# Kernel optimization log

Measured on AMD Instinct MI355X. Metric: run time of the kernel, lower is better.

Reference implementation:

```python
import jax, jax.numpy as jnp
import numpy as np
from jax import lax

FREQ, TIME = 8, 8
TSLOTS, NUM_AP = 8, 4
N_DEV = 8192
E_DD, E_DA, E_AD = 262144, 32768, 32768
HID = 64


def _w(key, shape):
    fan_in = shape[0] if len(shape) == 2 else int(np.prod(shape[1:]))
    return jax.random.normal(key, shape, jnp.float32) / np.sqrt(fan_in)


def setup_inputs() -> dict:
    key = jax.random.key(0)
    ks = iter(jax.random.split(key, 64))
    inp = {}
    inp['device_pos'] = jax.random.normal(next(ks), (N_DEV, 2), jnp.float32)
    inp['ap_pos'] = jax.random.normal(next(ks), (NUM_AP, 2), jnp.float32)
    inp['csi'] = jax.random.normal(next(ks), (N_DEV, NUM_AP, FREQ, TIME, 2), jnp.float32)
    inp['node_packets'] = jax.random.randint(next(ks), (N_DEV,), 0, 100, jnp.int32)
    inp['dd_src'] = jax.random.randint(next(ks), (E_DD,), 0, N_DEV, jnp.int32)
    inp['dd_dst'] = jax.random.randint(next(ks), (E_DD,), 0, N_DEV, jnp.int32)
    inp['da_src'] = jax.random.randint(next(ks), (E_DA,), 0, N_DEV, jnp.int32)
    inp['da_dst'] = jax.random.randint(next(ks), (E_DA,), 0, NUM_AP, jnp.int32)
    inp['ad_src'] = jax.random.randint(next(ks), (E_AD,), 0, NUM_AP, jnp.int32)
    inp['ad_dst'] = jax.random.randint(next(ks), (E_AD,), 0, N_DEV, jnp.int32)
    # CSIEncoder params
    inp['cnn1_W'] = _w(next(ks), (16, 2, 3, 3)); inp['cnn1_b'] = jnp.zeros((16,), jnp.float32)
    inp['cnn2_W'] = _w(next(ks), (32, 16, 3, 3)); inp['cnn2_b'] = jnp.zeros((32,), jnp.float32)
    inp['csi_fc_W'] = _w(next(ks), (32 * FREQ * TIME, HID)); inp['csi_fc_b'] = jnp.zeros((HID,), jnp.float32)
    # DeviceEncoder params
    inp['dev_pos_W'] = _w(next(ks), (3, 16)); inp['dev_pos_b'] = jnp.zeros((16,), jnp.float32)
    inp['dev_csi_W'] = _w(next(ks), (NUM_AP * HID, 64)); inp['dev_csi_b'] = jnp.zeros((64,), jnp.float32)
    inp['dev_merge_W'] = _w(next(ks), (80, 64)); inp['dev_merge_b'] = jnp.zeros((64,), jnp.float32)
    # APEncoder params
    inp['ap_enc_W'] = _w(next(ks), (2, 64)); inp['ap_enc_b'] = jnp.zeros((64,), jnp.float32)
    # 2 hetero layers x 3 relations GraphConv(64,64)
    for name in ['g1_dd', 'g1_da', 'g1_ad', 'g2_dd', 'g2_da', 'g2_ad']:
        inp[name + '_W'] = _w(next(ks), (64, 64))
        inp[name + '_b'] = jnp.zeros((64,), jnp.float32)
    # ap_head (sched_head is defined but unused in the original forward)
    inp['aph1_W'] = _w(next(ks), (64, 64)); inp['aph1_b'] = jnp.zeros((64,), jnp.float32)
    inp['aph2_W'] = _w(next(ks), (64, TSLOTS * NUM_AP)); inp['aph2_b'] = jnp.zeros((TSLOTS * NUM_AP,), jnp.float32)
    return inp


def _conv2d(x, W, b):
    y = lax.conv_general_dilated(x, W, (1, 1), 'SAME', dimension_numbers=('NCHW', 'OIHW', 'NCHW'))
    return y + b[None, :, None, None]


def _graph_conv(x_src, src, dst, n_src, n_dst, W, b):
    # DGL GraphConv, norm='both': x/sqrt(out_deg) -> scatter-sum -> /sqrt(in_deg) -> linear
    ones = jnp.ones(src.shape[0], x_src.dtype)
    deg_out = jnp.maximum(jax.ops.segment_sum(ones, src, num_segments=n_src), 1.0)
    deg_in = jnp.maximum(jax.ops.segment_sum(ones, dst, num_segments=n_dst), 1.0)
    m = (x_src * lax.rsqrt(deg_out)[:, None])[src]            # gather per edge
    agg = jax.ops.segment_sum(m, dst, num_segments=n_dst)      # scatter-sum to dst
    agg = agg * lax.rsqrt(deg_in)[:, None]
    return agg @ W + b


def reference(device_pos, ap_pos, csi, node_packets, dd_src, dd_dst, da_src, da_dst, ad_src, ad_dst,
              cnn1_W, cnn1_b, cnn2_W, cnn2_b, csi_fc_W, csi_fc_b,
              dev_pos_W, dev_pos_b, dev_csi_W, dev_csi_b, dev_merge_W, dev_merge_b,
              ap_enc_W, ap_enc_b,
              g1_dd_W, g1_dd_b, g1_da_W, g1_da_b, g1_ad_W, g1_ad_b,
              g2_dd_W, g2_dd_b, g2_da_W, g2_da_b, g2_ad_W, g2_ad_b,
              aph1_W, aph1_b, aph2_W, aph2_b):
    N, AP = csi.shape[0], csi.shape[1]
    # CSIEncoder (per-AP loop vectorized as a single batched conv over N*AP)
    x = csi.reshape(N * AP, FREQ, TIME, 2).transpose(0, 3, 1, 2)   # [N*AP,2,F,T]
    x = jax.nn.relu(_conv2d(x, cnn1_W, cnn1_b))
    x = jax.nn.relu(_conv2d(x, cnn2_W, cnn2_b))
    x = x.reshape(N * AP, -1)                                      # [N*AP, 32*F*T]
    csi_embed = jax.nn.relu(x @ csi_fc_W + csi_fc_b).reshape(N, AP * HID)
    # DeviceEncoder
    pin = jnp.concatenate([device_pos, node_packets.astype(jnp.float32)[:, None]], axis=1)
    pos_f = jax.nn.relu(pin @ dev_pos_W + dev_pos_b)
    csi_f = jax.nn.relu(csi_embed @ dev_csi_W + dev_csi_b)
    h_dev = jax.nn.relu(jnp.concatenate([pos_f, csi_f], axis=1) @ dev_merge_W + dev_merge_b)
    # APEncoder
    h_ap = jax.nn.relu(ap_pos @ ap_enc_W + ap_enc_b)
    # HeteroGraphConv layer 1 (aggregate='sum' across relations sharing dst type)
    hd1 = (_graph_conv(h_dev, dd_src, dd_dst, N, N, g1_dd_W, g1_dd_b)
           + _graph_conv(h_ap, ad_src, ad_dst, NUM_AP, N, g1_ad_W, g1_ad_b))
    ha1 = _graph_conv(h_dev, da_src, da_dst, N, NUM_AP, g1_da_W, g1_da_b)
    hd1, ha1 = jax.nn.relu(hd1), jax.nn.relu(ha1)
    # HeteroGraphConv layer 2
    hd2 = (_graph_conv(hd1, dd_src, dd_dst, N, N, g2_dd_W, g2_dd_b)
           + _graph_conv(ha1, ad_src, ad_dst, NUM_AP, N, g2_ad_W, g2_ad_b))
    hd2 = jax.nn.relu(hd2)
    # ap_head -> [N, T, A]
    ap_logits = (jax.nn.relu(hd2 @ aph1_W + aph1_b) @ aph2_W + aph2_b).reshape(N, TSLOTS, NUM_AP)
    logits_AP = ap_logits.transpose(2, 1, 0)                       # [A,T,N]
    # eval branch: deterministic softmax + argmax one-hot over devices
    ap_soft_AP = jax.nn.softmax(logits_AP, axis=-1)
    idx = jnp.argmax(logits_AP, axis=-1)                           # [A,T]
    ap_onehot_AP = jax.nn.one_hot(idx, N, dtype=logits_AP.dtype)   # [A,T,N]
    ap_onehot_final = ap_onehot_AP.transpose(2, 1, 0)              # [N,T,A]
    sched_soft = ap_soft_AP.sum(axis=0).T                          # [N,T]
    sched_hard = (ap_onehot_final.sum(axis=-1) > 0).astype(jnp.float32)
    return (sched_hard, ap_logits, sched_soft)
```

## Files before the change

kernel.cpp:

```cpp
#include <hip/hip_runtime.h>

#define NDEV 8192
#define NAP  4
#define NSAMP 32768
#define EDD 262144
#define EDA 32768
#define EAD 32768
#define CHUNK 8192
#define KC 128
#define ASTR2 132

typedef float vf2 __attribute__((ext_vector_type(2)));
static __device__ __forceinline__ vf2 pk_fma(vf2 a, vf2 b, vf2 c) {
    return __builtin_elementwise_fma(a, b, c);
}

using sh8 = __attribute__((ext_vector_type(8))) short;
using f32x4 = __attribute__((ext_vector_type(4))) float;
using f32x16 = __attribute__((ext_vector_type(16))) float;

static __device__ __forceinline__ unsigned short bf16_rtne(float f) {
    unsigned u = __float_as_uint(f);
    u += 0x7fffu + ((u >> 16) & 1u);
    return (unsigned short)(u >> 16);
}
static __device__ __forceinline__ float bf16f(unsigned short h) {
    return __uint_as_float(((unsigned)h) << 16);
}

__global__ void repack_kernel(const float* __restrict__ w2, float* __restrict__ wpk,
                              const float* __restrict__ w1, float* __restrict__ w1p,
                              const float* __restrict__ fcW, uint4* __restrict__ wfc,
                              const float* __restrict__ Wc, uint4* __restrict__ wcc)
{
    int i = blockIdx.x * 256 + threadIdx.x;
    if (i < 1152) {
        int lane = i & 63, s = (i >> 6) & 1, tap = i >> 7;
        int oc = lane & 31, g = lane >> 5;
        unsigned int d[4];
        #pragma unroll
        for (int d4 = 0; d4 < 4; ++d4) {
            unsigned short u01[2];
            #pragma unroll
            for (int h = 0; h < 2; ++h) {
                int e = 2 * d4 + h;
                int ic = g * 8 + e;
                float v = w2[oc * 144 + ic * 9 + tap];
                unsigned short hi = bf16_rtne(v);
                u01[h] = (s == 0) ? hi : bf16_rtne(v - bf16f(hi));
            }
            d[d4] = (unsigned)u01[0] | ((unsigned)u01[1] << 16);
        }
        ((uint4*)wpk)[i] = make_uint4(d[0], d[1], d[2], d[3]);
    }
    int j = i - 4608;
    if (j >= 0 && j < 288) {
        int h = j & 1, v = j >> 1;
        int o2 = v & 7, r = v >> 3;
        w1p[j] = w1[(2 * o2 + h) * 18 + r];
    }
    int h1 = i - 5120;
    if (h1 >= 0 && h1 < 32768) {
        int s = h1 & 1, l = (h1 >> 1) & 63, nt = (h1 >> 7) & 3, kstep = h1 >> 9;
        unsigned int d[4];
        #pragma unroll
        for (int d4 = 0; d4 < 4; ++d4) {
            unsigned short u01[2];
            #pragma unroll
            for (int hh = 0; hh < 2; ++hh) {
                int e = 2 * d4 + hh;
                int k = kstep * 32 + (l >> 4) * 8 + e;
                int n = nt * 16 + (l & 15);
                float v = fcW[(long)k * 64 + n];
                unsigned short hi = bf16_rtne(v);
                u01[hh] = (s == 0) ? hi : bf16_rtne(v - bf16f(hi));
            }
            d[d4] = (unsigned)u01[0] | ((unsigned)u01[1] << 16);
        }
        wfc[h1] = make_uint4(d[0], d[1], d[2], d[3]);
    }
    int h2 = i - 37888;
    if (h2 >= 0 && h2 < 4096) {
        int s = h2 & 1, l = (h2 >> 1) & 63, nt = (h2 >> 7) & 3, kstep = h2 >> 9;
        unsigned int d[4];
        #pragma unroll
        for (int d4 = 0; d4 < 4; ++d4) {
            unsigned short u01[2];
            #pragma unroll
            for (int hh = 0; hh < 2; ++hh) {
                int e = 2 * d4 + hh;
                int k = kstep * 32 + (l >> 4) * 8 + e;
                int n = nt * 16 + (l & 15);
                float v = Wc[(long)k * 64 + n];
                unsigned short hi = bf16_rtne(v);
                u01[hh] = (s == 0) ? hi : bf16_rtne(v - bf16f(hi));
            }
            d[d4] = (unsigned)u01[0] | ((unsigned)u01[1] << 16);
        }
        wcc[h2] = make_uint4(d[0], d[1], d[2], d[3]);
    }
}

__global__ __launch_bounds__(256) void conv_kernel(
    const float* __restrict__ csi,
    float* __restrict__ c2,
    const float* __restrict__ w1p, const float* __restrict__ b1,
    const float* __restrict__ wpk, const float* __restrict__ b2)
{
    __shared__ float sw1p[288];
    __shared__ float sb1[16];
    __shared__ float sb2[32];
    __shared__ float inpad[4][2][10][10];
    __shared__ __align__(16) unsigned short c1h[15360];
    const int tid = threadIdx.x;

    for (int i = tid; i < 288; i += 256) sw1p[i] = w1p[i];
    if (tid < 16) sb1[tid] = b1[tid];
    if (tid < 32) sb2[tid] = b2[tid];
    float* ip = &inpad[0][0][0][0];
    for (int i = tid; i < 800; i += 256) ip[i] = 0.f;
    unsigned int* cz = (unsigned int*)c1h;
    for (int i = tid; i < 7680; i += 256) cz[i] = 0u;
    __syncthreads();

    const long s0 = (long)blockIdx.x * 4;
    for (int i = tid; i < 512; i += 256) {
        int si = i >> 7, r = i & 127;
        int f = r >> 4, t = (r >> 1) & 7, c = r & 1;
        inpad[si][c][f + 1][t + 1] = csi[s0 * 128 + i];
    }
    __syncthreads();

    {
        const int si1 = tid >> 6, p1 = tid & 63;
        const int f1 = p1 >> 3, t1 = p1 & 7;
        float inv[18];
        #pragma unroll
        for (int ic = 0; ic < 2; ++ic)
            #pragma unroll
            for (int df = 0; df < 3; ++df)
                #pragma unroll
                for (int dt = 0; dt < 3; ++dt)
                    inv[ic * 9 + df * 3 + dt] = inpad[si1][ic][f1 + df][t1 + dt];
        vf2 a1[8];
        #pragma unroll
        for (int o2 = 0; o2 < 8; ++o2) a1[o2] = (vf2){sb1[2 * o2], sb1[2 * o2 + 1]};
        const vf2* sw1v = (const vf2*)sw1p;
        #pragma unroll
        for (int r = 0; r < 18; ++r) {
            vf2 xv = {inv[r], inv[r]};
            #pragma unroll
            for (int o2 = 0; o2 < 8; ++o2)
                a1[o2] = pk_fma(xv, sw1v[r * 8 + o2], a1[o2]);
        }
        float v[16];
        #pragma unroll
        for (int o2 = 0; o2 < 8; ++o2) {
            v[2 * o2]     = fmaxf(a1[o2].x, 0.f);
            v[2 * o2 + 1] = fmaxf(a1[o2].y, 0.f);
        }
        const int cell = ((f1 + 1) * 12 + (t1 + 1)) * 8;
        #pragma unroll
        for (int g = 0; g < 2; ++g) {
            unsigned int hd[4], ld[4];
            #pragma unroll
            for (int d = 0; d < 4; ++d) {
                float x0 = v[g * 8 + 2 * d], x1 = v[g * 8 + 2 * d + 1];
                unsigned short h0 = bf16_rtne(x0), h1 = bf16_rtne(x1);
                unsigned short l0 = bf16_rtne(x0 - bf16f(h0));
                unsigned short l1 = bf16_rtne(x1 - bf16f(h1));
                hd[d] = (unsigned)h0 | ((unsigned)h1 << 16);
                ld[d] = (unsigned)l0 | ((unsigned)l1 << 16);
            }
            *(uint4*)&c1h[(si1 * 4 + g) * 960 + cell]     = make_uint4(hd[0], hd[1], hd[2], hd[3]);
            *(uint4*)&c1h[(si1 * 4 + 2 + g) * 960 + cell] = make_uint4(ld[0], ld[1], ld[2], ld[3]);
        }
    }

    const int lane = tid & 63;
    sh8 Bh[9], Bl[9];
    {
        const sh8* bfp = (const sh8*)wpk;
        #pragma unroll
        for (int tap = 0; tap < 9; ++tap) {
            Bh[tap] = bfp[(tap * 2 + 0) * 64 + lane];
            Bl[tap] = bfp[(tap * 2 + 1) * 64 + lane];
        }
    }
    __syncthreads();

    const int w = __builtin_amdgcn_readfirstlane(tid >> 6);
    const int rr = lane & 31, g = lane >> 5;
    const float bias = sb2[rr];
    f32x16 acc0, acc1;
    #pragma unroll
    for (int u = 0; u < 16; ++u) { acc0[u] = bias; acc1[u] = bias; }

    const int p0f = rr >> 3, pt = rr & 7;
    const int p1f = 4 + p0f;
    const int hb = (w * 4 + g) * 960;
    const int lb = (w * 4 + 2 + g) * 960;

    #pragma unroll
    for (int df = 0; df < 3; ++df) {
        #pragma unroll
        for (int dt = 0; dt < 3; ++dt) {
            const int tap = df * 3 + dt;
            const int c0 = ((p0f + df) * 12 + (pt + dt)) * 8;
            const int c1i = ((p1f + df) * 12 + (pt + dt)) * 8;
            sh8 Ah0 = *(const sh8*)&c1h[hb + c0];
            sh8 Al0 = *(const sh8*)&c1h[lb + c0];
            sh8 Ah1 = *(const sh8*)&c1h[hb + c1i];
            sh8 Al1 = *(const sh8*)&c1h[lb + c1i];
            acc0 = __builtin_amdgcn_mfma_f32_32x32x16_bf16(Ah0, Bh[tap], acc0, 0, 0, 0);
            acc1 = __builtin_amdgcn_mfma_f32_32x32x16_bf16(Ah1, Bh[tap], acc1, 0, 0, 0);
            acc0 = __builtin_amdgcn_mfma_f32_32x32x16_bf16(Ah0, Bl[tap], acc0, 0, 0, 0);
            acc1 = __builtin_amdgcn_mfma_f32_32x32x16_bf16(Ah1, Bl[tap], acc1, 0, 0, 0);
            acc0 = __builtin_amdgcn_mfma_f32_32x32x16_bf16(Al0, Bh[tap], acc0, 0, 0, 0);
            acc1 = __builtin_amdgcn_mfma_f32_32x32x16_bf16(Al1, Bh[tap], acc1, 0, 0, 0);
        }
    }

    float* cb = &c2[(s0 + w) * 2048 + (long)rr * 64];
    #pragma unroll
    for (int qq = 0; qq < 4; ++qq) {
        float4 o;
        o.x = fmaxf(acc0[4 * qq + 0], 0.f); o.y = fmaxf(acc0[4 * qq + 1], 0.f);
        o.z = fmaxf(acc0[4 * qq + 2], 0.f); o.w = fmaxf(acc0[4 * qq + 3], 0.f);
        *(float4*)&cb[8 * qq + 4 * g] = o;
    }
    #pragma unroll
    for (int qq = 0; qq < 4; ++qq) {
        float4 o;
        o.x = fmaxf(acc1[4 * qq + 0], 0.f); o.y = fmaxf(acc1[4 * qq + 1], 0.f);
        o.z = fmaxf(acc1[4 * qq + 2], 0.f); o.w = fmaxf(acc1[4 * qq + 3], 0.f);
        *(float4*)&cb[32 + 8 * qq + 4 * g] = o;
    }
}

__global__ __launch_bounds__(256) void fc16_kernel(
    const float* __restrict__ A, const uint4* __restrict__ Wfrag,
    const float* __restrict__ bias, float* __restrict__ out, int K)
{
    __shared__ __align__(16) float smem[4224];
    float* As = smem;
    const int tid = threadIdx.x;
    const long m0g = (long)blockIdx.x * 16;
    const int ks = tid >> 6;
    const int lane = tid & 63;
    const int mrow = lane & 15;
    const int g = lane >> 4;

    f32x4 acc[4];
    #pragma unroll
    for (int nt = 0; nt < 4; ++nt) acc[nt] = (f32x4){0.f, 0.f, 0.f, 0.f};

    for (int kc = 0; kc < K; kc += KC) {
        __syncthreads();
        #pragma unroll
        for (int i = 0; i < 2; ++i) {
            int idx = tid + i * 256;
            int m = idx >> 5, kq = idx & 31;
            float4 v = *(const float4*)&A[(m0g + m) * K + kc + kq * 4];
            *(float4*)&As[m * ASTR2 + kq * 4] = v;
        }
        __syncthreads();
        const int kstep = (kc >> 5) + ks;
        const uint4* bp = Wfrag + (size_t)kstep * 512 + lane * 2;
        uint4 bh0 = bp[0],   bl0 = bp[1];
        uint4 bh1 = bp[128], bl1 = bp[129];
        uint4 bh2 = bp[256], bl2 = bp[257];
        uint4 bh3 = bp[384], bl3 = bp[385];
        const float4 a0 = *(const float4*)&As[mrow * ASTR2 + ks * 32 + g * 8];
        const float4 a1 = *(const float4*)&As[mrow * ASTR2 + ks * 32 + g * 8 + 4];
        float av[8] = {a0.x, a0.y, a0.z, a0.w, a1.x, a1.y, a1.z, a1.w};
        unsigned short hs[8], lss[8];
        #pragma unroll
        for (int e = 0; e < 8; ++e) {
            hs[e] = bf16_rtne(av[e]);
            lss[e] = bf16_rtne(av[e] - bf16f(hs[e]));
        }
        sh8 Ah = {(short)hs[0], (short)hs[1], (short)hs[2], (short)hs[3],
                  (short)hs[4], (short)hs[5], (short)hs[6], (short)hs[7]};
        sh8 Al = {(short)lss[0], (short)lss[1], (short)lss[2], (short)lss[3],
                  (short)lss[4], (short)lss[5], (short)lss[6], (short)lss[7]};
        #define FCMM(ntv, bhv, blv) \
            acc[ntv] = __builtin_amdgcn_mfma_f32_16x16x32_bf16(Ah, *(const sh8*)&(bhv), acc[ntv], 0, 0, 0); \
            acc[ntv] = __builtin_amdgcn_mfma_f32_16x16x32_bf16(Ah, *(const sh8*)&(blv), acc[ntv], 0, 0, 0); \
            acc[ntv] = __builtin_amdgcn_mfma_f32_16x16x32_bf16(Al, *(const sh8*)&(bhv), acc[ntv], 0, 0, 0);
        FCMM(0, bh0, bl0)
        FCMM(1, bh1, bl1)
        FCMM(2, bh2, bl2)
        FCMM(3, bh3, bl3)
        #undef FCMM
    }
    __syncthreads();
    float* red = smem;
    #pragma unroll
    for (int nt = 0; nt < 4; ++nt)
        #pragma unroll
        for (int r = 0; r < 4; ++r)
            red[(ks * 16 + g * 4 + r) * 64 + nt * 16 + mrow] = acc[nt][r];
    __syncthreads();
    {
        int m = tid >> 4, oq = tid & 15;
        float4 r0 = *(float4*)&red[(0 * 16 + m) * 64 + oq * 4];
        float4 r1 = *(float4*)&red[(1 * 16 + m) * 64 + oq * 4];
        float4 r2 = *(float4*)&red[(2 * 16 + m) * 64 + oq * 4];
        float4 r3 = *(float4*)&red[(3 * 16 + m) * 64 + oq * 4];
        const float4 b4 = *(const float4*)&bias[oq * 4];
        float4 o4;
        o4.x = fmaxf(r0.x + r1.x + r2.x + r3.x + b4.x, 0.f);
        o4.y = fmaxf(r0.y + r1.y + r2.y + r3.y + b4.y, 0.f);
        o4.z = fmaxf(r0.z + r1.z + r2.z + r3.z + b4.z, 0.f);
        o4.w = fmaxf(r0.w + r1.w + r2.w + r3.w + b4.w, 0.f);
        *(float4*)&out[(m0g + m) * 64 + oq * 4] = o4;
    }
}

__global__ __launch_bounds__(256) void merge_kernel(
    const float* __restrict__ dpos, const int* __restrict__ pkts,
    const float* __restrict__ csif,
    const float* __restrict__ Wp, const float* __restrict__ bp,
    const float* __restrict__ Wm, const float* __restrict__ bm,
    const int* __restrict__ degout,
    float* __restrict__ hdev, float* __restrict__ xn,
    const float* __restrict__ appos, const float* __restrict__ Wap,
    const float* __restrict__ bap, const int* __restrict__ degapo,
    float* __restrict__ hap, float* __restrict__ xnap)
{
    __shared__ float sWm[80][64];
    __shared__ float spos[4][16];
    __shared__ float scf[4][64];
    const int tid = threadIdx.x;
    for (int i = tid; i < 5120; i += 256) sWm[i >> 6][i & 63] = Wm[i];
    const int n0 = blockIdx.x * 4;
    (&scf[0][0])[tid] = csif[(long)n0 * 64 + tid];
    if (tid < 64) {
        int dl = tid >> 4, o = tid & 15;
        int d = n0 + dl;
        float px = dpos[d * 2], py = dpos[d * 2 + 1], pk = (float)pkts[d];
        float v = bp[o] + px * Wp[o] + py * Wp[16 + o] + pk * Wp[32 + o];
        spos[dl][o] = fmaxf(v, 0.f);
    }
    __syncthreads();
    const int o = tid & 63, dl = tid >> 6;
    float h = bm[o];
    #pragma unroll
    for (int j = 0; j < 16; ++j) h += spos[dl][j] * sWm[j][o];
    #pragma unroll 8
    for (int j = 0; j < 64; ++j) h += scf[dl][j] * sWm[16 + j][o];
    h = fmaxf(h, 0.f);
    const long idx = (long)(n0 + dl) * 64 + o;
    hdev[idx] = h;
    xn[idx] = h * rsqrtf(fmaxf((float)degout[n0 + dl], 1.f));
    if (blockIdx.x == 0) {
        int a = tid >> 6, oo = tid & 63;
        float v = fmaxf(bap[oo] + appos[a * 2] * Wap[oo] + appos[a * 2 + 1] * Wap[64 + oo], 0.f);
        hap[tid] = v;
        xnap[tid] = v * rsqrtf(fmaxf((float)degapo[a], 1.f));
    }
}

__global__ __launch_bounds__(256) void degrees_kernel(
    const int* __restrict__ dd_src, const int* __restrict__ dd_dst,
    const int* __restrict__ da_src, const int* __restrict__ da_dst,
    const int* __restrict__ ad_src, const int* __restrict__ ad_dst,
    int* deg_dd_out, int* deg_dd_in, int* deg_da_out, int* deg_ad_in, int* deg_small)
{
    __shared__ int s4[16];
    const int tid = threadIdx.x;
    if (tid < 16) s4[tid] = 0;
    __syncthreads();
    const int gid = blockIdx.x * 256 + tid;
    atomicAdd(&deg_dd_out[dd_src[gid]], 1);
    atomicAdd(&deg_dd_in[dd_dst[gid]], 1);
    if (gid < EDA) {
        atomicAdd(&deg_da_out[da_src[gid]], 1);
        atomicAdd(&s4[da_dst[gid]], 1);
        atomicAdd(&s4[8 + ad_src[gid]], 1);
        atomicAdd(&deg_ad_in[ad_dst[gid]], 1);
    }
    __syncthreads();
    if (tid < 16 && s4[tid] != 0) atomicAdd(&deg_small[tid], s4[tid]);
}

__global__ __launch_bounds__(1024) void scan_kernel(
    const int* __restrict__ degA, int* rsA, int* curA,
    const int* __restrict__ degB, int* rsB, int* curB)
{
    const int* deg = blockIdx.x ? degB : degA;
    int* rs = blockIdx.x ? rsB : rsA;
    int* cur = blockIdx.x ? curB : curA;
    __shared__ int sd[1024];
    const int tid = threadIdx.x;
    const int base = tid * 8;
    int v[8]; int s = 0;
    #pragma unroll
    for (int j = 0; j < 8; ++j) { v[j] = deg[base + j]; s += v[j]; }
    sd[tid] = s;
    __syncthreads();
    for (int off = 1; off < 1024; off <<= 1) {
        int t = (tid >= off) ? sd[tid - off] : 0;
        __syncthreads();
        sd[tid] += t;
        __syncthreads();
    }
    int ex = sd[tid] - s;
    #pragma unroll
    for (int j = 0; j < 8; ++j) { rs[base + j] = ex; cur[base + j] = ex; ex += v[j]; }
}

__global__ __launch_bounds__(256) void reorder_kernel(
    const int* __restrict__ src, const int* __restrict__ dst,
    int* __restrict__ cursor, int* __restrict__ ssrc, int nE)
{
    int e = blockIdx.x * 256 + threadIdx.x;
    if (e < nE) {
        int pos = atomicAdd(&cursor[dst[e]], 1);
        ssrc[pos] = src[e];
    }
}

__global__ __launch_bounds__(256) void gatherx_kernel(
    const int* __restrict__ rsdd, const int* __restrict__ degddi,
    const int* __restrict__ ssdd, const float* __restrict__ xn, float* __restrict__ aggdd,
    const int* __restrict__ rsad, const int* __restrict__ degadi,
    const int* __restrict__ ssad, const float* __restrict__ xnap, float* __restrict__ aggad,
    const int* __restrict__ da_src, const int* __restrict__ da_dst,
    const float* __restrict__ hdev, const int* __restrict__ degdao,
    float* __restrict__ aggda)
{
    __shared__ float sacc[4][64];
    const int b = blockIdx.x;
    const int tid = threadIdx.x;
    if (b < 1024) {
        const bool isdd = b < 512;
        const int lane = tid & 63;
        const int gbase = lane & 48;
        const int lg = lane & 15;
        const int fq = lg * 4;
        const int d = (isdd ? b : b - 512) * 16 + (tid >> 4);
        const int* rs = isdd ? rsdd : rsad;
        const int* dg = isdd ? degddi : degadi;
        const int* ss = isdd ? ssdd : ssad;
        const float* x = isdd ? xn : xnap;
        float* agg = isdd ? aggdd : aggad;
        const int start = rs[d], len = dg[d];
        float ax = 0.f, ay = 0.f, az = 0.f, aw = 0.f;
        for (int j = 0; j < len; j += 16) {
            const int rem = min(16, len - j);
            const int myidx = ss[start + j + min(lg, rem - 1)];
            float4 v[16];
            #pragma unroll
            for (int k = 0; k < 16; ++k) {
                const int sk = __shfl(myidx, gbase + min(k, rem - 1), 64);
                v[k] = *(const float4*)&x[(long)sk * 64 + fq];
            }
            #pragma unroll
            for (int k = 0; k < 16; ++k) {
                const float m = (k < rem) ? 1.f : 0.f;
                ax += m * v[k].x; ay += m * v[k].y;
                az += m * v[k].z; aw += m * v[k].w;
            }
        }
        const float sc = rsqrtf(fmaxf((float)len, 1.f));
        float4 o;
        o.x = ax * sc; o.y = ay * sc; o.z = az * sc; o.w = aw * sc;
        *(float4*)&agg[(long)d * 64 + fq] = o;
    } else {
        (&sacc[0][0])[tid] = 0.f;
        __syncthreads();
        const int f = tid & 63;
        const int base = (b - 1024) * 128;
        for (int e = base + (tid >> 6); e < base + 128; e += 4) {
            int s = da_src[e], d = da_dst[e];
            float sc = rsqrtf(fmaxf((float)degdao[s], 1.f));
            atomicAdd(&sacc[d][f], hdev[(long)s * 64 + f] * sc);
        }
        __syncthreads();
        float v = (&sacc[0][0])[tid];
        if (v != 0.f) atomicAdd(&aggda[tid], v);
    }
}

__global__ __launch_bounds__(256) void combinex_kernel(
    const float* __restrict__ agg1, const float* __restrict__ W1, const float* __restrict__ b1,
    const float* __restrict__ agg2, const float* __restrict__ W2, const float* __restrict__ b2,
    const int* __restrict__ degout, float* __restrict__ out, float* __restrict__ xnout,
    const float* __restrict__ aggda, const int* __restrict__ degdai,
    const float* __restrict__ Wda, const float* __restrict__ bda,
    const int* __restrict__ degapo, float* __restrict__ ha_out, float* __restrict__ ha_xn)
{
    __shared__ float sW1[64][64];
    __shared__ float sW2[64][64];
    __shared__ float sa1[4][64];
    __shared__ float sa2[4][64];
    const int tid = threadIdx.x;
    if (blockIdx.x < 2048) {
        for (int i = tid; i < 4096; i += 256) { sW1[i >> 6][i & 63] = W1[i]; sW2[i >> 6][i & 63] = W2[i]; }
        const int n0 = blockIdx.x * 4;
        (&sa1[0][0])[tid] = agg1[(long)n0 * 64 + tid];
        (&sa2[0][0])[tid] = agg2[(long)n0 * 64 + tid];
        __syncthreads();
        const int o = tid & 63, dl = tid >> 6;
        float acc1 = 0.f, acc2 = 0.f;
        #pragma unroll 8
        for (int k = 0; k < 64; ++k) {
            acc1 += sa1[dl][k] * sW1[k][o];
            acc2 += sa2[dl][k] * sW2[k][o];
        }
        float h = fmaxf(acc1 + acc2 + b1[o] + b2[o], 0.f);
        const long idx = (long)(n0 + dl) * 64 + o;
        out[idx] = h;
        if (xnout) xnout[idx] = h * rsqrtf(fmaxf((float)degout[n0 + dl], 1.f));
    } else {
        const int o = tid & 63, a = tid >> 6;
        float acc = 0.f;
        for (int k = 0; k < 64; ++k) acc += aggda[a * 64 + k] * Wda[k * 64 + o];
        float r = rsqrtf(fmaxf((float)degdai[a], 1.f));
        float h = fmaxf(acc * r + bda[o], 0.f);
        ha_out[tid] = h;
        ha_xn[tid] = h * rsqrtf(fmaxf((float)degapo[a], 1.f));
    }
}

__global__ __launch_bounds__(256) void head_kernel(
    const float* __restrict__ hd2,
    const float* __restrict__ W1, const float* __restrict__ b1,
    const float* __restrict__ W2, const float* __restrict__ b2,
    float* __restrict__ logits_out)
{
    __shared__ float sW1[64][64];
    __shared__ float sW2[64][32];
    __shared__ float sh[4][64];
    __shared__ float st[4][64];
    const int tid = threadIdx.x;
    for (int i = tid; i < 4096; i += 256) sW1[i >> 6][i & 63] = W1[i];
    for (int i = tid; i < 2048; i += 256) sW2[i >> 5][i & 31] = W2[i];
    const int n0 = blockIdx.x * 4;
    (&sh[0][0])[tid] = hd2[(long)n0 * 64 + tid];
    __syncthreads();
    const int o = tid & 63, dl = tid >> 6;
    float acc = b1[o];
    #pragma unroll 8
    for (int k = 0; k < 64; ++k) acc += sh[dl][k] * sW1[k][o];
    st[dl][o] = fmaxf(acc, 0.f);
    __syncthreads();
    if (tid < 128) {
        int j = tid & 31, d2 = tid >> 5;
        float a2 = b2[j];
        #pragma unroll 8
        for (int k = 0; k < 64; ++k) a2 += st[d2][k] * sW2[k][j];
        logits_out[(long)(n0 + d2) * 32 + j] = a2;
    }
}

__global__ __launch_bounds__(1024) void softmax_stats_kernel(
    const float* __restrict__ logits,
    float* __restrict__ smax, int* __restrict__ sargm, float* __restrict__ ssum)
{
    __shared__ float smx[1024];
    __shared__ int sid[1024];
    __shared__ float ssm[1024];
    const int j = blockIdx.x;
    const int tid = threadIdx.x;
    float best = -__builtin_inff(); int bid = 0x7fffffff;
    for (int n = tid; n < NDEV; n += 1024) {
        float v = logits[n * 32 + j];
        if (v > best) { best = v; bid = n; }
    }
    smx[tid] = best; sid[tid] = bid;
    __syncthreads();
    for (int s = 512; s > 0; s >>= 1) {
        if (tid < s) {
            float v2 = smx[tid + s]; int i2 = sid[tid + s];
            if (v2 > smx[tid] || (v2 == smx[tid] && i2 < sid[tid])) { smx[tid] = v2; sid[tid] = i2; }
        }
        __syncthreads();
    }
    const float mx = smx[0];
    float part = 0.f;
    for (int n = tid; n < NDEV; n += 1024) part += expf(logits[n * 32 + j] - mx);
    ssm[tid] = part;
    __syncthreads();
    for (int s = 512; s > 0; s >>= 1) {
        if (tid < s) ssm[tid] += ssm[tid + s];
        __syncthreads();
    }
    if (tid == 0) { smax[j] = mx; sargm[j] = sid[0]; ssum[j] = ssm[0]; }
}

__global__ __launch_bounds__(256) void final_kernel(
    const float* __restrict__ logits, const float* __restrict__ smax,
    const int* __restrict__ sargm, const float* __restrict__ ssum,
    float* __restrict__ hard, float* __restrict__ soft)
{
    const int gid = blockIdx.x * 256 + threadIdx.x;
    const int n = gid >> 3, t = gid & 7;
    float s = 0.f; int h = 0;
    #pragma unroll
    for (int a = 0; a < 4; ++a) {
        int j = t * 4 + a;
        s += expf(logits[n * 32 + j] - smax[j]) / ssum[j];
        h |= (sargm[j] == n) ? 1 : 0;
    }
    hard[gid] = (float)h;
    soft[gid] = s;
}

extern "C" void kernel_launch(void* const* d_in, const int* in_sizes, int n_in,
                              void* d_out, int out_size, void* d_ws, size_t ws_size,
                              hipStream_t stream)
{
    const float* device_pos = (const float*)d_in[0];
    const float* ap_pos     = (const float*)d_in[1];
    const float* csi        = (const float*)d_in[2];
    const int*   node_pk    = (const int*)d_in[3];
    const int* dd_src = (const int*)d_in[4];
    const int* dd_dst = (const int*)d_in[5];
    const int* da_src = (const int*)d_in[6];
    const int* da_dst = (const int*)d_in[7];
    const int* ad_src = (const int*)d_in[8];
    const int* ad_dst = (const int*)d_in[9];
    const float* w1  = (const float*)d_in[10]; const float* b1  = (const float*)d_in[11];
    const float* w2  = (const float*)d_in[12]; const float* b2  = (const float*)d_in[13];
    const float* fcW = (const float*)d_in[14]; const float* fcb = (const float*)d_in[15];
    const float* Wp  = (const float*)d_in[16]; const float* bp  = (const float*)d_in[17];
    const float* Wc  = (const float*)d_in[18]; const float* bc  = (const float*)d_in[19];
    const float* Wm  = (const float*)d_in[20]; const float* bm  = (const float*)d_in[21];
    const float* Wap = (const float*)d_in[22]; const float* bap = (const float*)d_in[23];
    const float* g1ddW = (const float*)d_in[24]; const float* g1ddb = (const float*)d_in[25];
    const float* g1daW = (const float*)d_in[26]; const float* g1dab = (const float*)d_in[27];
    const float* g1adW = (const float*)d_in[28]; const float* g1adb = (const float*)d_in[29];
    const float* g2ddW = (const float*)d_in[30]; const float* g2ddb = (const float*)d_in[31];
    const float* g2adW = (const float*)d_in[34]; const float* g2adb = (const float*)d_in[35];
    const float* a1W = (const float*)d_in[36]; const float* a1b = (const float*)d_in[37];
    const float* a2W = (const float*)d_in[38]; const float* a2b = (const float*)d_in[39];

    float* ws = (float*)d_ws;
    size_t o_c2    = 0;
    size_t o_emb   = o_c2 + (size_t)CHUNK * 2048;
    size_t o_csif  = o_emb + (size_t)NSAMP * 64;
    size_t o_hdev  = o_csif + (size_t)NDEV * 64;
    size_t o_hap   = o_hdev + (size_t)NDEV * 64;
    size_t o_hd1   = o_hap + 256;
    size_t o_ha1   = o_hd1 + (size_t)NDEV * 64;
    size_t o_hd2   = o_ha1 + 256;
    size_t o_aggdd = o_hd2 + (size_t)NDEV * 64;
    size_t o_aggad = o_aggdd + (size_t)NDEV * 64;
    size_t o_xn    = o_aggad + (size_t)NDEV * 64;
    size_t o_xnap  = o_xn + (size_t)NDEV * 64;
    size_t o_wpk   = o_xnap + 256;
    size_t o_w1p   = o_wpk + 4608;
    size_t o_wfc   = o_w1p + 288;
    size_t o_wcc   = o_wfc + 131072;
    size_t o_zero  = o_wcc + 16384;
    size_t o_degddo = o_zero;
    size_t o_degddi = o_degddo + NDEV;
    size_t o_degdao = o_degddi + NDEV;
    size_t o_degadi = o_degdao + NDEV;
    size_t o_degsm  = o_degadi + NDEV;
    size_t o_aggda  = o_degsm + 16;
    size_t o_zend   = o_aggda + 256;
    size_t o_rsdd  = o_zend;
    size_t o_curdd = o_rsdd + NDEV;
    size_t o_rsad  = o_curdd + NDEV;
    size_t o_curad = o_rsad + NDEV;
    size_t o_ssdd  = o_curad + NDEV;
    size_t o_ssad  = o_ssdd + EDD;
    size_t o_smax  = o_ssad + EAD;
    size_t o_ssum  = o_smax + 32;
    size_t o_sargm = o_ssum + 32;

    float* out = (float*)d_out;
    float* out_hard   = out;
    float* out_logits = out + 65536;
    float* out_soft   = out + 65536 + 262144;

    hipMemsetAsync((void*)(ws + o_zero), 0, (o_zend - o_zero) * sizeof(float), stream);
    repack_kernel<<<164, 256, 0, stream>>>(w2, ws + o_wpk, w1, ws + o_w1p,
                                           fcW, (uint4*)(ws + o_wfc),
                                           Wc, (uint4*)(ws + o_wcc));

    degrees_kernel<<<EDD / 256, 256, 0, stream>>>(dd_src, dd_dst, da_src, da_dst, ad_src, ad_dst,
                                                  (int*)(ws + o_degddo), (int*)(ws + o_degddi),
                                                  (int*)(ws + o_degdao), (int*)(ws + o_degadi),
                                                  (int*)(ws + o_degsm));
    scan_kernel<<<2, 1024, 0, stream>>>((int*)(ws + o_degddi), (int*)(ws + o_rsdd), (int*)(ws + o_curdd),
                                        (int*)(ws + o_degadi), (int*)(ws + o_rsad), (int*)(ws + o_curad));
    reorder_kernel<<<EDD / 256, 256, 0, stream>>>(dd_src, dd_dst, (int*)(ws + o_curdd),
                                                  (int*)(ws + o_ssdd), EDD);
    reorder_kernel<<<EAD / 256, 256, 0, stream>>>(ad_src, ad_dst, (int*)(ws + o_curad),
                                                  (int*)(ws + o_ssad), EAD);

    for (int c = 0; c < NSAMP / CHUNK; ++c) {
        const float* csi_c = csi + (size_t)c * CHUNK * 128;
        float* emb_c = ws + o_emb + (size_t)c * CHUNK * 64;
        conv_kernel<<<CHUNK / 4, 256, 0, stream>>>(csi_c, ws + o_c2, ws + o_w1p, b1, ws + o_wpk, b2);
        fc16_kernel<<<CHUNK / 16, 256, 0, stream>>>(ws + o_c2, (const uint4*)(ws + o_wfc),
                                                    fcb, emb_c, 2048);
    }

    fc16_kernel<<<NDEV / 16, 256, 0, stream>>>(ws + o_emb, (const uint4*)(ws + o_wcc),
                                               bc, ws + o_csif, 256);
    merge_kernel<<<NDEV / 4, 256, 0, stream>>>(device_pos, node_pk, ws + o_csif,
                                               Wp, bp, Wm, bm, (int*)(ws + o_degddo),
                                               ws + o_hdev, ws + o_xn,
                                               ap_pos, Wap, bap, (int*)(ws + o_degsm) + 8,
                                               ws + o_hap, ws + o_xnap);

    gatherx_kernel<<<1280, 256, 0, stream>>>((int*)(ws + o_rsdd), (int*)(ws + o_degddi),
                                             (int*)(ws + o_ssdd), ws + o_xn, ws + o_aggdd,
                                             (int*)(ws + o_rsad), (int*)(ws + o_degadi),
                                             (int*)(ws + o_ssad), ws + o_xnap, ws + o_aggad,
                                             da_src, da_dst, ws + o_hdev,
                                             (int*)(ws + o_degdao), ws + o_aggda);
    combinex_kernel<<<2049, 256, 0, stream>>>(ws + o_aggdd, g1ddW, g1ddb,
                                              ws + o_aggad, g1adW, g1adb,
                                              (int*)(ws + o_degddo), ws + o_hd1, ws + o_xn,
                                              ws + o_aggda, (int*)(ws + o_degsm),
                                              g1daW, g1dab, (int*)(ws + o_degsm) + 8,
                                              ws + o_ha1, ws + o_xnap);

    gatherx_kernel<<<1024, 256, 0, stream>>>((int*)(ws + o_rsdd), (int*)(ws + o_degddi),
                                             (int*)(ws + o_ssdd), ws + o_xn, ws + o_aggdd,
                                             (int*)(ws + o_rsad), (int*)(ws + o_degadi),
                                             (int*)(ws + o_ssad), ws + o_xnap, ws + o_aggad,
                                             da_src, da_dst, ws + o_hd1,
                                             (int*)(ws + o_degdao), ws + o_aggda);
    combinex_kernel<<<2048, 256, 0, stream>>>(ws + o_aggdd, g2ddW, g2ddb,
                                              ws + o_aggad, g2adW, g2adb,
                                              (int*)(ws + o_degddo), ws + o_hd2, nullptr,
                                              nullptr, nullptr, nullptr, nullptr,
                                              nullptr, nullptr, nullptr);

    head_kernel<<<NDEV / 4, 256, 0, stream>>>(ws + o_hd2, a1W, a1b, a2W, a2b, out_logits);

    softmax_stats_kernel<<<32, 1024, 0, stream>>>(out_logits, ws + o_smax,
                                                  (int*)(ws + o_sargm), ws + o_ssum);
    final_kernel<<<65536 / 256, 256, 0, stream>>>(out_logits, ws + o_smax,
                                                  (int*)(ws + o_sargm), ws + o_ssum,
                                                  out_hard, out_soft);
    (void)in_sizes; (void)n_in; (void)out_size; (void)ws_size;
}
```

Baseline: 516.4 us.

## Fuse CSI conv and FC layers into one kernel keeping conv output in LDS

Replaces the chunked conv_kernel and fc16_kernel launches with a single convfc kernel. Each 512-thread block handles 16 samples, keeps the conv2 activations in a large shared-memory buffer in position-major layout, and runs the 2048x64 FC with split-K across waves followed by an LDS reduction. The FC weight repack is permuted to match the new activation layout. This removes the global round trip of the 2048-wide intermediate and several launches, at the cost of about 135KB of LDS per block, which limits occupancy to one block per CU.

```diff
diff --git a/kernel.cpp b/kernel.cpp
--- a/kernel.cpp
+++ b/kernel.cpp
@@ -6,7 +6,6 @@
 #define EDD 262144
 #define EDA 32768
 #define EAD 32768
-#define CHUNK 8192
 #define KC 128
 #define ASTR2 132
 
@@ -69,9 +68,10 @@
             #pragma unroll
             for (int hh = 0; hh < 2; ++hh) {
                 int e = 2 * d4 + hh;
-                int k = kstep * 32 + (l >> 4) * 8 + e;
+                int kp = kstep * 32 + (l >> 4) * 8 + e;
+                int korig = (kp & 31) * 64 + (kp >> 5);
                 int n = nt * 16 + (l & 15);
-                float v = fcW[(long)k * 64 + n];
+                float v = fcW[(long)korig * 64 + n];
                 unsigned short hi = bf16_rtne(v);
                 u01[hh] = (s == 0) ? hi : bf16_rtne(v - bf16f(hi));
             }
@@ -101,38 +101,52 @@
     }
 }
 
-__global__ __launch_bounds__(256) void conv_kernel(
+#define C2STR 2052
+__global__ __launch_bounds__(512) void convfc_kernel(
     const float* __restrict__ csi,
-    float* __restrict__ c2,
     const float* __restrict__ w1p, const float* __restrict__ b1,
-    const float* __restrict__ wpk, const float* __restrict__ b2)
-{
+    const float* __restrict__ wpk, const float* __restrict__ b2,
+    const uint4* __restrict__ wfc, const float* __restrict__ fcb,
+    float* __restrict__ emb)
+{
+    __shared__ __align__(16) char smem[135680];
     __shared__ float sw1p[288];
     __shared__ float sb1[16];
     __shared__ float sb2[32];
-    __shared__ float inpad[4][2][10][10];
-    __shared__ __align__(16) unsigned short c1h[15360];
+    __shared__ float sbF[64];
+    float* inpad = (float*)smem;
+    unsigned short* c1h = (unsigned short*)(smem + 12800);
+    float* c2h = (float*)smem;
+    float* red = (float*)smem;
     const int tid = threadIdx.x;
-
-    for (int i = tid; i < 288; i += 256) sw1p[i] = w1p[i];
+    const int lane = tid & 63;
+    const int w = __builtin_amdgcn_readfirstlane(tid >> 6);
+
+    for (int i = tid; i < 288; i += 512) sw1p[i] = w1p[i];
     if (tid < 16) sb1[tid] = b1[tid];
     if (tid < 32) sb2[tid] = b2[tid];
-    float* ip = &inpad[0][0][0][0];
-    for (int i = tid; i < 800; i += 256) ip[i] = 0.f;
-    unsigned int* cz = (unsigned int*)c1h;
-    for (int i = tid; i < 7680; i += 256) cz[i] = 0u;
-    __syncthreads();
-
-    const long s0 = (long)blockIdx.x * 4;
-    for (int i = tid; i < 512; i += 256) {
+    if (tid < 64) sbF[tid] = fcb[tid];
+    {
+        const uint4 z4 = make_uint4(0u, 0u, 0u, 0u);
+        uint4* ip4 = (uint4*)inpad;
+        for (int i = tid; i < 800; i += 512) ip4[i] = z4;
+        uint4* c14 = (uint4*)c1h;
+        for (int i = tid; i < 15360; i += 512) c14[i] = z4;
+    }
+    __syncthreads();
+
+    const long s0 = (long)blockIdx.x * 16;
+    for (int i = tid; i < 2048; i += 512) {
         int si = i >> 7, r = i & 127;
         int f = r >> 4, t = (r >> 1) & 7, c = r & 1;
-        inpad[si][c][f + 1][t + 1] = csi[s0 * 128 + i];
-    }
-    __syncthreads();
-
-    {
-        const int si1 = tid >> 6, p1 = tid & 63;
+        inpad[si * 200 + c * 100 + (f + 1) * 10 + (t + 1)] = csi[s0 * 128 + i];
+    }
+    __syncthreads();
+
+    #pragma unroll
+    for (int it = 0; it < 2; ++it) {
+        const int si1 = it * 8 + w;
+        const int p1 = lane;
         const int f1 = p1 >> 3, t1 = p1 & 7;
         float inv[18];
         #pragma unroll
@@ -141,7 +155,8 @@
             for (int df = 0; df < 3; ++df)
                 #pragma unroll
                 for (int dt = 0; dt < 3; ++dt)
-                    inv[ic * 9 + df * 3 + dt] = inpad[si1][ic][f1 + df][t1 + dt];
+                    inv[ic * 9 + df * 3 + dt] =
+                        inpad[si1 * 200 + ic * 100 + (f1 + df) * 10 + (t1 + dt)];
         vf2 a1[8];
         #pragma unroll
         for (int o2 = 0; o2 < 8; ++o2) a1[o2] = (vf2){sb1[2 * o2], sb1[2 * o2 + 1]};
@@ -177,7 +192,6 @@
         }
     }
 
-    const int lane = tid & 63;
     sh8 Bh[9], Bl[9];
     {
         const sh8* bfp = (const sh8*)wpk;
@@ -189,52 +203,106 @@
     }
     __syncthreads();
 
-    const int w = __builtin_amdgcn_readfirstlane(tid >> 6);
     const int rr = lane & 31, g = lane >> 5;
-    const float bias = sb2[rr];
-    f32x16 acc0, acc1;
-    #pragma unroll
-    for (int u = 0; u < 16; ++u) { acc0[u] = bias; acc1[u] = bias; }
-
+    const float bias2 = sb2[rr];
     const int p0f = rr >> 3, pt = rr & 7;
     const int p1f = 4 + p0f;
-    const int hb = (w * 4 + g) * 960;
-    const int lb = (w * 4 + 2 + g) * 960;
-
-    #pragma unroll
-    for (int df = 0; df < 3; ++df) {
-        #pragma unroll
-        for (int dt = 0; dt < 3; ++dt) {
-            const int tap = df * 3 + dt;
-            const int c0 = ((p0f + df) * 12 + (pt + dt)) * 8;
-            const int c1i = ((p1f + df) * 12 + (pt + dt)) * 8;
-            sh8 Ah0 = *(const sh8*)&c1h[hb + c0];
-            sh8 Al0 = *(const sh8*)&c1h[lb + c0];
-            sh8 Ah1 = *(const sh8*)&c1h[hb + c1i];
-            sh8 Al1 = *(const sh8*)&c1h[lb + c1i];
-            acc0 = __builtin_amdgcn_mfma_f32_32x32x16_bf16(Ah0, Bh[tap], acc0, 0, 0, 0);
-            acc1 = __builtin_amdgcn_mfma_f32_32x32x16_bf16(Ah1, Bh[tap], acc1, 0, 0, 0);
-            acc0 = __builtin_amdgcn_mfma_f32_32x32x16_bf16(Ah0, Bl[tap], acc0, 0, 0, 0);
-            acc1 = __builtin_amdgcn_mfma_f32_32x32x16_bf16(Ah1, Bl[tap], acc1, 0, 0, 0);
-            acc0 = __builtin_amdgcn_mfma_f32_32x32x16_bf16(Al0, Bh[tap], acc0, 0, 0, 0);
-            acc1 = __builtin_amdgcn_mfma_f32_32x32x16_bf16(Al1, Bh[tap], acc1, 0, 0, 0);
-        }
-    }
-
-    float* cb = &c2[(s0 + w) * 2048 + (long)rr * 64];
-    #pragma unroll
-    for (int qq = 0; qq < 4; ++qq) {
-        float4 o;
-        o.x = fmaxf(acc0[4 * qq + 0], 0.f); o.y = fmaxf(acc0[4 * qq + 1], 0.f);
-        o.z = fmaxf(acc0[4 * qq + 2], 0.f); o.w = fmaxf(acc0[4 * qq + 3], 0.f);
-        *(float4*)&cb[8 * qq + 4 * g] = o;
-    }
-    #pragma unroll
-    for (int qq = 0; qq < 4; ++qq) {
-        float4 o;
-        o.x = fmaxf(acc1[4 * qq + 0], 0.f); o.y = fmaxf(acc1[4 * qq + 1], 0.f);
-        o.z = fmaxf(acc1[4 * qq + 2], 0.f); o.w = fmaxf(acc1[4 * qq + 3], 0.f);
-        *(float4*)&cb[32 + 8 * qq + 4 * g] = o;
+    #pragma unroll
+    for (int q = 0; q < 2; ++q) {
+        const int s = q * 8 + w;
+        f32x16 acc0, acc1;
+        #pragma unroll
+        for (int u = 0; u < 16; ++u) { acc0[u] = bias2; acc1[u] = bias2; }
+        const int hb = (s * 4 + g) * 960;
+        const int lb = (s * 4 + 2 + g) * 960;
+        #pragma unroll
+        for (int df = 0; df < 3; ++df) {
+            #pragma unroll
+            for (int dt = 0; dt < 3; ++dt) {
+                const int tap = df * 3 + dt;
+                const int c0 = ((p0f + df) * 12 + (pt + dt)) * 8;
+                const int c1i = ((p1f + df) * 12 + (pt + dt)) * 8;
+                sh8 Ah0 = *(const sh8*)&c1h[hb + c0];
+                sh8 Al0 = *(const sh8*)&c1h[lb + c0];
+                sh8 Ah1 = *(const sh8*)&c1h[hb + c1i];
+                sh8 Al1 = *(const sh8*)&c1h[lb + c1i];
+                acc0 = __builtin_amdgcn_mfma_f32_32x32x16_bf16(Ah0, Bh[tap], acc0, 0, 0, 0);
+                acc1 = __builtin_amdgcn_mfma_f32_32x32x16_bf16(Ah1, Bh[tap], acc1, 0, 0, 0);
+                acc0 = __builtin_amdgcn_mfma_f32_32x32x16_bf16(Ah0, Bl[tap], acc0, 0, 0, 0);
+                acc1 = __builtin_amdgcn_mfma_f32_32x32x16_bf16(Ah1, Bl[tap], acc1, 0, 0, 0);
+                acc0 = __builtin_amdgcn_mfma_f32_32x32x16_bf16(Al0, Bh[tap], acc0, 0, 0, 0);
+                acc1 = __builtin_amdgcn_mfma_f32_32x32x16_bf16(Al1, Bh[tap], acc1, 0, 0, 0);
+            }
+        }
+        __syncthreads();
+        float* crow = c2h + (size_t)s * C2STR;
+        #pragma unroll
+        for (int i = 0; i < 16; ++i) {
+            const int pos = (i & 3) + 8 * (i >> 2) + 4 * g;
+            crow[pos * 32 + rr]        = fmaxf(acc0[i], 0.f);
+            crow[(pos + 32) * 32 + rr] = fmaxf(acc1[i], 0.f);
+        }
+    }
+    __syncthreads();
+
+    const int ks = w;
+    const int mrow = lane & 15;
+    const int g2 = lane >> 4;
+    f32x4 acc[4];
+    #pragma unroll
+    for (int nt = 0; nt < 4; ++nt) acc[nt] = (f32x4){0.f, 0.f, 0.f, 0.f};
+    #pragma unroll 2
+    for (int t = 0; t < 8; ++t) {
+        const int kstep = ks * 8 + t;
+        const uint4* bp = wfc + (size_t)kstep * 512 + lane * 2;
+        uint4 bh0 = bp[0],   bl0 = bp[1];
+        uint4 bh1 = bp[128], bl1 = bp[129];
+        uint4 bh2 = bp[256], bl2 = bp[257];
+        uint4 bh3 = bp[384], bl3 = bp[385];
+        const float4 a0 = *(const float4*)&c2h[mrow * C2STR + kstep * 32 + g2 * 8];
+        const float4 a1 = *(const float4*)&c2h[mrow * C2STR + kstep * 32 + g2 * 8 + 4];
+        float av[8] = {a0.x, a0.y, a0.z, a0.w, a1.x, a1.y, a1.z, a1.w};
+        unsigned short hs[8], lss[8];
+        #pragma unroll
+        for (int e = 0; e < 8; ++e) {
+            hs[e] = bf16_rtne(av[e]);
+            lss[e] = bf16_rtne(av[e] - bf16f(hs[e]));
+        }
+        sh8 Ah = {(short)hs[0], (short)hs[1], (short)hs[2], (short)hs[3],
+                  (short)hs[4], (short)hs[5], (short)hs[6], (short)hs[7]};
+        sh8 Al = {(short)lss[0], (short)lss[1], (short)lss[2], (short)lss[3],
+                  (short)lss[4], (short)lss[5], (short)lss[6], (short)lss[7]};
+        #define FCMM(ntv, bhv, blv) \
+            acc[ntv] = __builtin_amdgcn_mfma_f32_16x16x32_bf16(Ah, *(const sh8*)&(bhv), acc[ntv], 0, 0, 0); \
+            acc[ntv] = __builtin_amdgcn_mfma_f32_16x16x32_bf16(Ah, *(const sh8*)&(blv), acc[ntv], 0, 0, 0); \
+            acc[ntv] = __builtin_amdgcn_mfma_f32_16x16x32_bf16(Al, *(const sh8*)&(bhv), acc[ntv], 0, 0, 0);
+        FCMM(0, bh0, bl0)
+        FCMM(1, bh1, bl1)
+        FCMM(2, bh2, bl2)
+        FCMM(3, bh3, bl3)
+        #undef FCMM
+    }
+    __syncthreads();
+    #pragma unroll
+    for (int nt = 0; nt < 4; ++nt)
+        #pragma unroll
+        for (int r = 0; r < 4; ++r)
+            red[(ks * 16 + g2 * 4 + r) * 64 + nt * 16 + mrow] = acc[nt][r];
+    __syncthreads();
+    if (tid < 256) {
+        const int m = tid >> 4, oq = tid & 15;
+        float4 sum;
+        sum.x = sbF[oq * 4 + 0]; sum.y = sbF[oq * 4 + 1];
+        sum.z = sbF[oq * 4 + 2]; sum.w = sbF[oq * 4 + 3];
+        #pragma unroll
+        for (int jq = 0; jq < 8; ++jq) {
+            float4 rv = *(float4*)&red[(jq * 16 + m) * 64 + oq * 4];
+            sum.x += rv.x; sum.y += rv.y; sum.z += rv.z; sum.w += rv.w;
+        }
+        float4 o4;
+        o4.x = fmaxf(sum.x, 0.f); o4.y = fmaxf(sum.y, 0.f);
+        o4.z = fmaxf(sum.z, 0.f); o4.w = fmaxf(sum.w, 0.f);
+        *(float4*)&emb[(s0 + m) * 64 + oq * 4] = o4;
     }
 }
 
@@ -639,8 +707,7 @@
     const float* a2W = (const float*)d_in[38]; const float* a2b = (const float*)d_in[39];
 
     float* ws = (float*)d_ws;
-    size_t o_c2    = 0;
-    size_t o_emb   = o_c2 + (size_t)CHUNK * 2048;
+    size_t o_emb   = 0;
     size_t o_csif  = o_emb + (size_t)NSAMP * 64;
     size_t o_hdev  = o_csif + (size_t)NDEV * 64;
     size_t o_hap   = o_hdev + (size_t)NDEV * 64;
@@ -694,13 +761,8 @@
     reorder_kernel<<<EAD / 256, 256, 0, stream>>>(ad_src, ad_dst, (int*)(ws + o_curad),
                                                   (int*)(ws + o_ssad), EAD);
 
-    for (int c = 0; c < NSAMP / CHUNK; ++c) {
-        const float* csi_c = csi + (size_t)c * CHUNK * 128;
-        float* emb_c = ws + o_emb + (size_t)c * CHUNK * 64;
-        conv_kernel<<<CHUNK / 4, 256, 0, stream>>>(csi_c, ws + o_c2, ws + o_w1p, b1, ws + o_wpk, b2);
-        fc16_kernel<<<CHUNK / 16, 256, 0, stream>>>(ws + o_c2, (const uint4*)(ws + o_wfc),
-                                                    fcb, emb_c, 2048);
-    }
+    convfc_kernel<<<NSAMP / 16, 512, 0, stream>>>(csi, ws + o_w1p, b1, ws + o_wpk, b2,
+                                                  (const uint4*)(ws + o_wfc), fcb, ws + o_emb);
 
     fc16_kernel<<<NDEV / 16, 256, 0, stream>>>(ws + o_emb, (const uint4*)(ws + o_wcc),
                                                bc, ws + o_csif, 256);
```

After: 434.7 us. 1.19x faster.
